# Kernel optimization log

Hardware: AMD Instinct MI355X
Metric: run time of the kernel (lower is better)

The kernel has to match this reference:

```python
import jax, jax.numpy as jnp
import numpy as np

B, S, D, H, DFF, PDIM = 16, 1024, 256, 8, 1024, 64
N = B * S
E = 262144
DH = D // H
EPS = 1e-5


def _ln(x, w=None, b=None):
    mu = jnp.mean(x, axis=-1, keepdims=True)
    var = jnp.mean((x - mu) ** 2, axis=-1, keepdims=True)
    xn = (x - mu) * jax.lax.rsqrt(var + EPS)
    if w is not None:
        xn = xn * w + b
    return xn


def setup_inputs() -> dict:
    key = jax.random.key(0)
    ks = jax.random.split(key, 24)
    sc = lambda *s: 0.02
    inp = {
        "x": jax.random.normal(ks[0], (B, S, D), jnp.float32),
        "prop_cond": jax.random.normal(ks[1], (B, PDIM), jnp.float32),
        "edge_index": jax.random.randint(ks[2], (2, E), 0, N, jnp.int64),
        # AdaLN 1 & 2
        "ada1_gw": jax.random.normal(ks[3], (D, PDIM)) * 0.02,
        "ada1_gb": jnp.ones((D,), jnp.float32),
        "ada1_bw": jax.random.normal(ks[4], (D, PDIM)) * 0.02,
        "ada1_bb": jnp.zeros((D,), jnp.float32),
        "ada2_gw": jax.random.normal(ks[5], (D, PDIM)) * 0.02,
        "ada2_gb": jnp.ones((D,), jnp.float32),
        "ada2_bw": jax.random.normal(ks[6], (D, PDIM)) * 0.02,
        "ada2_bb": jnp.zeros((D,), jnp.float32),
        # LayerNorms
        "ln1_w": jnp.ones((D,), jnp.float32), "ln1_b": jnp.zeros((D,), jnp.float32),
        "ln2_w": jnp.ones((D,), jnp.float32), "ln2_b": jnp.zeros((D,), jnp.float32),
        "gln_w": jnp.ones((D,), jnp.float32), "gln_b": jnp.zeros((D,), jnp.float32),
        # MHA
        "in_proj_w": jax.random.normal(ks[7], (3 * D, D)) * 0.02,
        "in_proj_b": jnp.zeros((3 * D,), jnp.float32),
        "out_proj_w": jax.random.normal(ks[8], (D, D)) * 0.02,
        "out_proj_b": jnp.zeros((D,), jnp.float32),
        # FFN
        "ffn_w1": jax.random.normal(ks[9], (DFF, D)) * 0.02,
        "ffn_b1": jnp.zeros((DFF,), jnp.float32),
        "ffn_w2": jax.random.normal(ks[10], (D, DFF)) * 0.02,
        "ffn_b2": jnp.zeros((D,), jnp.float32),
        # GATConv (heads=1, concat=False)
        "gat_w": jax.random.normal(ks[11], (D, D)) * 0.02,
        "gat_att_src": jax.random.normal(ks[12], (D,)) * 0.02,
        "gat_att_dst": jax.random.normal(ks[13], (D,)) * 0.02,
        "gat_bias": jnp.zeros((D,), jnp.float32),
    }
    return inp


def _forward(x, prop_cond, edge_index,
             ada1_gw, ada1_gb, ada1_bw, ada1_bb,
             ada2_gw, ada2_gb, ada2_bw, ada2_bb,
             ln1_w, ln1_b, ln2_w, ln2_b, gln_w, gln_b,
             in_proj_w, in_proj_b, out_proj_w, out_proj_b,
             ffn_w1, ffn_b1, ffn_w2, ffn_b2,
             gat_w, gat_att_src, gat_att_dst, gat_bias):
    # ---- AdaLN 1 + attention block ----
    residual = x
    gamma = (prop_cond @ ada1_gw.T + ada1_gb)[:, None, :]  # [B,1,D]
    beta = (prop_cond @ ada1_bw.T + ada1_bb)[:, None, :]
    xa = gamma * _ln(x) + beta
    xn = _ln(xa, ln1_w, ln1_b)
    qkv = xn @ in_proj_w.T + in_proj_b  # [B,S,3D]
    q, k, v = jnp.split(qkv, 3, axis=-1)
    q = q.reshape(B, S, H, DH)
    k = k.reshape(B, S, H, DH)
    v = v.reshape(B, S, H, DH)
    scores = jnp.einsum("bqhd,bkhd->bhqk", q, k) / jnp.sqrt(jnp.float32(DH))
    attn = jax.nn.softmax(scores, axis=-1)
    ao = jnp.einsum("bhqk,bkhd->bqhd", attn, v).reshape(B, S, D)
    ao = ao @ out_proj_w.T + out_proj_b
    x = residual + ao

    # ---- GATConv over flattened nodes (self-loops, leaky_relu 0.2) ----
    nodes = x.reshape(N, D)
    h = nodes @ gat_w.T  # [N,D]
    ar = jnp.arange(N, dtype=edge_index.dtype)
    src = jnp.concatenate([edge_index[0], ar])
    dst = jnp.concatenate([edge_index[1], ar])
    a_src = h @ gat_att_src  # [N]
    a_dst = h @ gat_att_dst
    e = jax.nn.leaky_relu(a_src[src] + a_dst[dst], 0.2)  # [E+N]
    m = jax.ops.segment_max(e, dst, num_segments=N)
    e = jnp.exp(e - m[dst])
    z = jax.ops.segment_sum(e, dst, num_segments=N)
    alpha = e / z[dst]
    agg = jax.ops.segment_sum(alpha[:, None] * h[src], dst, num_segments=N)
    gnn_out = (agg + gat_bias).reshape(B, S, D)
    x = x + gnn_out
    x = _ln(x, gln_w, gln_b)

    # ---- AdaLN 2 + FFN block ----
    residual = x
    gamma = (prop_cond @ ada2_gw.T + ada2_gb)[:, None, :]
    beta = (prop_cond @ ada2_bw.T + ada2_bb)[:, None, :]
    xa = gamma * _ln(x) + beta
    xn = _ln(xa, ln2_w, ln2_b)
    ff = jax.nn.gelu(xn @ ffn_w1.T + ffn_b1, approximate=False) @ ffn_w2.T + ffn_b2
    return residual + ff


def reference(x, prop_cond, edge_index,
              ada1_gw, ada1_gb, ada1_bw, ada1_bb,
              ada2_gw, ada2_gb, ada2_bw, ada2_bb,
              ln1_w, ln1_b, ln2_w, ln2_b, gln_w, gln_b,
              in_proj_w, in_proj_b, out_proj_w, out_proj_b,
              ffn_w1, ffn_b1, ffn_w2, ffn_b2,
              gat_w, gat_att_src, gat_att_dst, gat_bias):
    return _forward(x, prop_cond, edge_index,
                    ada1_gw, ada1_gb, ada1_bw, ada1_bb,
                    ada2_gw, ada2_gb, ada2_bw, ada2_bb,
                    ln1_w, ln1_b, ln2_w, ln2_b, gln_w, gln_b,
                    in_proj_w, in_proj_b, out_proj_w, out_proj_b,
                    ffn_w1, ffn_b1, ffn_w2, ffn_b2,
                    gat_w, gat_att_src, gat_att_dst, gat_bias)
```

## Files before the change

kernel.cpp:

```cpp
#include <hip/hip_runtime.h>
#include <cmath>

#define B_    16
#define S_    1024
#define D_    256
#define H_    8
#define DH_   32
#define DFF_  1024
#define PDIM_ 64
#define N_    (B_ * S_)
#define E_    262144
#define ETOT_ (E_ + N_)
#define EPS_  1e-5f

typedef __attribute__((ext_vector_type(8))) short bf16x8;
typedef __attribute__((ext_vector_type(4))) float f32x4;

__device__ __forceinline__ float wave_sum(float v) {
#pragma unroll
  for (int m = 1; m < 64; m <<= 1) v += __shfl_xor(v, m, 64);
  return v;
}
__device__ __forceinline__ float wave_max(float v) {
#pragma unroll
  for (int m = 1; m < 64; m <<= 1) v = fmaxf(v, __shfl_xor(v, m, 64));
  return v;
}

__device__ __forceinline__ unsigned short f2bf(float f) {
  unsigned int u = __float_as_uint(f);
  unsigned int r = u + 0x7fffu + ((u >> 16) & 1u);
  return (unsigned short)(r >> 16);
}
__device__ __forceinline__ float bf2f(unsigned short s) {
  return __uint_as_float(((unsigned int)s) << 16);
}
__device__ __forceinline__ void split4(float4 v, ushort4& hi, ushort4& lo) {
  unsigned short h;
  h = f2bf(v.x); hi.x = h; lo.x = f2bf(v.x - bf2f(h));
  h = f2bf(v.y); hi.y = h; lo.y = f2bf(v.y - bf2f(h));
  h = f2bf(v.z); hi.z = h; lo.z = f2bf(v.z - bf2f(h));
  h = f2bf(v.w); hi.w = h; lo.w = f2bf(v.w - bf2f(h));
}

__global__ __launch_bounds__(256) void gamma_beta_kernel(
    const float* __restrict__ pc,
    const float* __restrict__ g1w, const float* __restrict__ g1b,
    const float* __restrict__ b1w, const float* __restrict__ b1b,
    const float* __restrict__ g2w, const float* __restrict__ g2b,
    const float* __restrict__ b2w, const float* __restrict__ b2b,
    float* __restrict__ gamma1, float* __restrict__ beta1,
    float* __restrict__ gamma2, float* __restrict__ beta2) {
  int i = blockIdx.x * 256 + threadIdx.x;
  if (i >= B_ * D_) return;
  int b = i >> 8, d = i & 255;
  const float* p = pc + b * PDIM_;
  float s1 = 0.f, s2 = 0.f, s3 = 0.f, s4 = 0.f;
#pragma unroll 8
  for (int k = 0; k < PDIM_; ++k) {
    float pv = p[k];
    s1 += pv * g1w[d * PDIM_ + k];
    s2 += pv * b1w[d * PDIM_ + k];
    s3 += pv * g2w[d * PDIM_ + k];
    s4 += pv * b2w[d * PDIM_ + k];
  }
  gamma1[i] = s1 + g1b[d];
  beta1[i]  = s2 + b1b[d];
  gamma2[i] = s3 + g2b[d];
  beta2[i]  = s4 + b2b[d];
}

__global__ __launch_bounds__(256) void adaln_kernel(
    const float* __restrict__ x, const float* __restrict__ gamma,
    const float* __restrict__ beta, const float* __restrict__ lnw,
    const float* __restrict__ lnb, float* __restrict__ out) {
  int wid = threadIdx.x >> 6, lane = threadIdx.x & 63;
  int r = blockIdx.x * 4 + wid;
  int b = r >> 10;
  const int c = lane << 2;
  float4 v = *(const float4*)&x[(size_t)r * D_ + c];
  float sum = wave_sum(v.x + v.y + v.z + v.w);
  float mu = sum * (1.f / D_);
  float d0 = v.x - mu, d1 = v.y - mu, d2 = v.z - mu, d3 = v.w - mu;
  float sq = wave_sum(d0 * d0 + d1 * d1 + d2 * d2 + d3 * d3);
  float rs = rsqrtf(sq * (1.f / D_) + EPS_);
  float4 g  = *(const float4*)&gamma[b * D_ + c];
  float4 be = *(const float4*)&beta[b * D_ + c];
  float a0 = g.x * (d0 * rs) + be.x;
  float a1 = g.y * (d1 * rs) + be.y;
  float a2 = g.z * (d2 * rs) + be.z;
  float a3 = g.w * (d3 * rs) + be.w;
  float sum2 = wave_sum(a0 + a1 + a2 + a3);
  float mu2 = sum2 * (1.f / D_);
  float e0 = a0 - mu2, e1 = a1 - mu2, e2 = a2 - mu2, e3 = a3 - mu2;
  float sq2 = wave_sum(e0 * e0 + e1 * e1 + e2 * e2 + e3 * e3);
  float rs2 = rsqrtf(sq2 * (1.f / D_) + EPS_);
  float4 w  = *(const float4*)&lnw[c];
  float4 bb = *(const float4*)&lnb[c];
  float4 o;
  o.x = e0 * rs2 * w.x + bb.x;
  o.y = e1 * rs2 * w.y + bb.y;
  o.z = e2 * rs2 * w.z + bb.z;
  o.w = e3 * rs2 * w.w + bb.w;
  *(float4*)&out[(size_t)r * D_ + c] = o;
}

template <int EPI, int MS>
__global__ __launch_bounds__(256) void gemm_mfma_kernel(
    const float* __restrict__ A, const float* __restrict__ Wt,
    const float* __restrict__ bias, const float* __restrict__ R,
    float* __restrict__ C, int M, int Nc, int K) {
  __shared__ __align__(16) unsigned short Ah[MS * 32][40];
  __shared__ __align__(16) unsigned short Al[MS * 32][40];
  __shared__ __align__(16) unsigned short Bh[128][40];
  __shared__ __align__(16) unsigned short Bl[128][40];
  const int t = threadIdx.x;
  const int w = t >> 6, l = t & 63;
  const int lr = l & 15, lg = l >> 4;
  const int bm = blockIdx.y * (MS * 32), bn = blockIdx.x * 128;
  constexpr int SA = (MS == 4) ? 1 : 2;
  constexpr int NA = (MS == 4) ? 4 : 2;
  const int sra = t >> SA;
  const int ska = (t & ((1 << SA) - 1)) * (NA * 4);
  const int srb = t >> 1;
  const int skb = (t & 1) * 16;
  const float* Ap = A + (size_t)(bm + sra) * K + ska;
  const float* Bp = Wt + (size_t)(bn + srb) * K + skb;

  f32x4 acc[MS][4];
#pragma unroll
  for (int i = 0; i < MS; ++i)
#pragma unroll
    for (int j = 0; j < 4; ++j) acc[i][j] = (f32x4){0.f, 0.f, 0.f, 0.f};

  float4 ra[NA], rb[4];
#pragma unroll
  for (int c = 0; c < NA; ++c) ra[c] = *(const float4*)(Ap + c * 4);
#pragma unroll
  for (int c = 0; c < 4; ++c) rb[c] = *(const float4*)(Bp + c * 4);

  const int nk = K >> 5;
  for (int kt = 0; kt < nk; ++kt) {
    __syncthreads();
#pragma unroll
    for (int c = 0; c < NA; ++c) {
      ushort4 h4, l4;
      split4(ra[c], h4, l4);
      *(ushort4*)&Ah[sra][ska + c * 4] = h4;
      *(ushort4*)&Al[sra][ska + c * 4] = l4;
    }
#pragma unroll
    for (int c = 0; c < 4; ++c) {
      ushort4 h4, l4;
      split4(rb[c], h4, l4);
      *(ushort4*)&Bh[srb][skb + c * 4] = h4;
      *(ushort4*)&Bl[srb][skb + c * 4] = l4;
    }
    if (kt + 1 < nk) {
      Ap += 32;
      Bp += 32;
#pragma unroll
      for (int c = 0; c < NA; ++c) ra[c] = *(const float4*)(Ap + c * 4);
#pragma unroll
      for (int c = 0; c < 4; ++c) rb[c] = *(const float4*)(Bp + c * 4);
    }
    __syncthreads();
    bf16x8 bhj[4], blj[4];
#pragma unroll
    for (int j = 0; j < 4; ++j) {
      bhj[j] = *(const bf16x8*)&Bh[(w & 1) * 64 + j * 16 + lr][lg * 8];
      blj[j] = *(const bf16x8*)&Bl[(w & 1) * 64 + j * 16 + lr][lg * 8];
    }
#pragma unroll
    for (int i = 0; i < MS; ++i) {
      bf16x8 ahi = *(const bf16x8*)&Ah[(w >> 1) * (MS * 16) + i * 16 + lr][lg * 8];
      bf16x8 ali = *(const bf16x8*)&Al[(w >> 1) * (MS * 16) + i * 16 + lr][lg * 8];
#pragma unroll
      for (int j = 0; j < 4; ++j) {
        acc[i][j] = __builtin_amdgcn_mfma_f32_16x16x32_bf16(ahi, bhj[j], acc[i][j], 0, 0, 0);
        acc[i][j] = __builtin_amdgcn_mfma_f32_16x16x32_bf16(ali, bhj[j], acc[i][j], 0, 0, 0);
        acc[i][j] = __builtin_amdgcn_mfma_f32_16x16x32_bf16(ahi, blj[j], acc[i][j], 0, 0, 0);
      }
    }
  }
#pragma unroll
  for (int i = 0; i < MS; ++i) {
    const int m0 = bm + (w >> 1) * (MS * 16) + i * 16 + lg * 4;
#pragma unroll
    for (int j = 0; j < 4; ++j) {
      const int n = bn + (w & 1) * 64 + j * 16 + lr;
      const float bv = bias ? bias[n] : 0.f;
#pragma unroll
      for (int r = 0; r < 4; ++r) {
        const size_t idx = (size_t)(m0 + r) * Nc + n;
        float v = acc[i][j][r] + bv;
        if (EPI == 1) v = 0.5f * v * (1.f + erff(v * 0.7071067811865476f));
        if (EPI == 2) v += R[idx];
        C[idx] = v;
      }
    }
  }
}

__global__ __launch_bounds__(256) void attn_kernel(
    const float* __restrict__ qkv, float* __restrict__ ao) {
  __shared__ __align__(16) unsigned short Kh[64][40];
  __shared__ __align__(16) unsigned short Kl[64][40];
  __shared__ __align__(16) unsigned short VTh[32][72];
  __shared__ __align__(16) unsigned short VTl[32][72];
  __shared__ __align__(16) unsigned short Ph[4][16][72];
  __shared__ __align__(16) unsigned short Pl[4][16][72];

  const int t = threadIdx.x;
  const int w = t >> 6;
  const int l = t & 63;
  const int lq = l & 15;
  const int g = l >> 4;
  const int qt = blockIdx.x, h = blockIdx.y, b = blockIdx.z;
  const int qbase = qt * 256 + w * 64;

  const float QS = 0.2550332772677823f;

  bf16x8 qh[4], ql[4];
#pragma unroll
  for (int qs = 0; qs < 4; ++qs) {
    const size_t rowq =
        ((size_t)(b * S_ + qbase + qs * 16 + lq)) * 768 + h * DH_ + g * 8;
    float4 qa = *(const float4*)&qkv[rowq];
    float4 qb = *(const float4*)&qkv[rowq + 4];
    float qf[8] = {qa.x, qa.y, qa.z, qa.w, qb.x, qb.y, qb.z, qb.w};
#pragma unroll
    for (int j = 0; j < 8; ++j) {
      float f = qf[j] * QS;
      unsigned short hi = f2bf(f);
      qh[qs][j] = (short)hi;
      ql[qs][j] = (short)f2bf(f - bf2f(hi));
    }
  }

  f32x4 oacc[4][2];
  float mrun[4], lrun[4];
#pragma unroll
  for (int qs = 0; qs < 4; ++qs) {
    oacc[qs][0] = (f32x4){0.f, 0.f, 0.f, 0.f};
    oacc[qs][1] = (f32x4){0.f, 0.f, 0.f, 0.f};
    mrun[qs] = -1e30f;
    lrun[qs] = 0.f;
  }

  const int key_s = t >> 2;
  const int dg = t & 3;

  for (int kt = 0; kt < 16; ++kt) {
    __syncthreads();
    {
      const size_t rowb =
          ((size_t)(b * S_ + kt * 64 + key_s)) * 768 + h * DH_ + dg * 8;
      float4 ka = *(const float4*)&qkv[rowb + 256];
      float4 kb = *(const float4*)&qkv[rowb + 260];
      float4 va = *(const float4*)&qkv[rowb + 512];
      float4 vb = *(const float4*)&qkv[rowb + 516];
      ushort4 h0, h1, l0, l1;
      split4(ka, h0, l0);
      split4(kb, h1, l1);
      *(ushort4*)&Kh[key_s][dg * 8] = h0;
      *(ushort4*)&Kh[key_s][dg * 8 + 4] = h1;
      *(ushort4*)&Kl[key_s][dg * 8] = l0;
      *(ushort4*)&Kl[key_s][dg * 8 + 4] = l1;
      float vf[8] = {va.x, va.y, va.z, va.w, vb.x, vb.y, vb.z, vb.w};
#pragma unroll
      for (int j = 0; j < 8; ++j) {
        unsigned short vh = f2bf(vf[j]);
        VTh[dg * 8 + j][key_s] = vh;
        VTl[dg * 8 + j][key_s] = f2bf(vf[j] - bf2f(vh));
      }
    }
    __syncthreads();

    bf16x8 kfh[4], kfl[4];
#pragma unroll
    for (int i = 0; i < 4; ++i) {
      kfh[i] = *(const bf16x8*)&Kh[i * 16 + lq][g * 8];
      kfl[i] = *(const bf16x8*)&Kl[i * 16 + lq][g * 8];
    }

#pragma unroll
    for (int qs = 0; qs < 4; ++qs) {
      f32x4 s[4];
#pragma unroll
      for (int i = 0; i < 4; ++i) {
        f32x4 c = (f32x4){0.f, 0.f, 0.f, 0.f};
        c = __builtin_amdgcn_mfma_f32_16x16x32_bf16(kfh[i], qh[qs], c, 0, 0, 0);
        c = __builtin_amdgcn_mfma_f32_16x16x32_bf16(kfh[i], ql[qs], c, 0, 0, 0);
        c = __builtin_amdgcn_mfma_f32_16x16x32_bf16(kfl[i], qh[qs], c, 0, 0, 0);
        s[i] = c;
      }
      float pm = -1e30f;
#pragma unroll
      for (int i = 0; i < 4; ++i)
#pragma unroll
        for (int r = 0; r < 4; ++r) pm = fmaxf(pm, s[i][r]);
      pm = fmaxf(pm, __shfl_xor(pm, 16, 64));
      pm = fmaxf(pm, __shfl_xor(pm, 32, 64));
      float mnew = fmaxf(mrun[qs], pm);
      float rfac = exp2f(mrun[qs] - mnew);
      mrun[qs] = mnew;
      oacc[qs][0] *= rfac;
      oacc[qs][1] *= rfac;
      float lsum = 0.f;
#pragma unroll
      for (int i = 0; i < 4; ++i) {
        ushort4 hv, lv;
        unsigned short hr[4], lr4[4];
#pragma unroll
        for (int r = 0; r < 4; ++r) {
          float p = exp2f(s[i][r] - mnew);
          lsum += p;
          unsigned short ph = f2bf(p);
          hr[r] = ph;
          lr4[r] = f2bf(p - bf2f(ph));
        }
        hv.x = hr[0]; hv.y = hr[1]; hv.z = hr[2]; hv.w = hr[3];
        lv.x = lr4[0]; lv.y = lr4[1]; lv.z = lr4[2]; lv.w = lr4[3];
        *(ushort4*)&Ph[w][lq][i * 16 + g * 4] = hv;
        *(ushort4*)&Pl[w][lq][i * 16 + g * 4] = lv;
      }
      lsum += __shfl_xor(lsum, 16, 64);
      lsum += __shfl_xor(lsum, 32, 64);
      lrun[qs] = lrun[qs] * rfac + lsum;

#pragma unroll
      for (int kh2 = 0; kh2 < 2; ++kh2) {
        bf16x8 pb = *(const bf16x8*)&Ph[w][lq][kh2 * 32 + g * 8];
        bf16x8 pl = *(const bf16x8*)&Pl[w][lq][kh2 * 32 + g * 8];
#pragma unroll
        for (int d = 0; d < 2; ++d) {
          bf16x8 vh = *(const bf16x8*)&VTh[d * 16 + lq][kh2 * 32 + g * 8];
          bf16x8 vl = *(const bf16x8*)&VTl[d * 16 + lq][kh2 * 32 + g * 8];
          oacc[qs][d] = __builtin_amdgcn_mfma_f32_16x16x32_bf16(vh, pb, oacc[qs][d], 0, 0, 0);
          oacc[qs][d] = __builtin_amdgcn_mfma_f32_16x16x32_bf16(vh, pl, oacc[qs][d], 0, 0, 0);
          oacc[qs][d] = __builtin_amdgcn_mfma_f32_16x16x32_bf16(vl, pb, oacc[qs][d], 0, 0, 0);
        }
      }
    }
  }

#pragma unroll
  for (int qs = 0; qs < 4; ++qs) {
    float inv = 1.f / lrun[qs];
    const size_t orow =
        ((size_t)(b * S_ + qbase + qs * 16 + lq)) * D_ + h * DH_;
#pragma unroll
    for (int d = 0; d < 2; ++d) {
      float4 ov;
      ov.x = oacc[qs][d][0] * inv;
      ov.y = oacc[qs][d][1] * inv;
      ov.z = oacc[qs][d][2] * inv;
      ov.w = oacc[qs][d][3] * inv;
      *(float4*)&ao[orow + d * 16 + g * 4] = ov;
    }
  }
}

__global__ __launch_bounds__(256) void adot_kernel(
    const float* __restrict__ h, const float* __restrict__ att_src,
    const float* __restrict__ att_dst, float* __restrict__ a_src,
    float* __restrict__ a_dst) {
  int wid = threadIdx.x >> 6, lane = threadIdx.x & 63;
  int n = blockIdx.x * 4 + wid;
  const int c = lane << 2;
  float4 hv = *(const float4*)&h[(size_t)n * D_ + c];
  float4 as = *(const float4*)&att_src[c];
  float4 ad = *(const float4*)&att_dst[c];
  float s = hv.x * as.x + hv.y * as.y + hv.z * as.z + hv.w * as.w;
  float d = hv.x * ad.x + hv.y * ad.y + hv.z * ad.z + hv.w * ad.w;
  s = wave_sum(s);
  d = wave_sum(d);
  if (lane == 0) { a_src[n] = s; a_dst[n] = d; }
}

__global__ __launch_bounds__(256) void hist_kernel(
    const int* __restrict__ e_dst, int* __restrict__ counts) {
  int i = blockIdx.x * 256 + threadIdx.x;
  if (i >= ETOT_) return;
  int dst = (i < E_) ? e_dst[i] : (i - E_);
  atomicAdd(&counts[dst], 1);
}

__global__ __launch_bounds__(1024) void scan_kernel(
    const int* __restrict__ counts, int* __restrict__ offsets,
    int* __restrict__ cursor) {
  __shared__ int sums[1024];
  const int t = threadIdx.x;
  int local[16];
  int s = 0;
#pragma unroll
  for (int i = 0; i < 16; ++i) { local[i] = s; s += counts[t * 16 + i]; }
  sums[t] = s;
  __syncthreads();
  for (int off = 1; off < 1024; off <<= 1) {
    int v = (t >= off) ? sums[t - off] : 0;
    __syncthreads();
    sums[t] += v;
    __syncthreads();
  }
  int base = (t > 0) ? sums[t - 1] : 0;
#pragma unroll
  for (int i = 0; i < 16; ++i) {
    int o = base + local[i];
    offsets[t * 16 + i] = o;
    cursor[t * 16 + i] = o;
  }
  if (t == 1023) offsets[N_] = sums[1023];
}

__global__ __launch_bounds__(256) void scatter_kernel(
    const int* __restrict__ e_src, const int* __restrict__ e_dst,
    int* __restrict__ cursor, int* __restrict__ csr_src) {
  int i = blockIdx.x * 256 + threadIdx.x;
  if (i >= ETOT_) return;
  int s = (i < E_) ? e_src[i] : (i - E_);
  int d = (i < E_) ? e_dst[i] : (i - E_);
  int slot = atomicAdd(&cursor[d], 1);
  csr_src[slot] = s;
}

__global__ __launch_bounds__(256) void gat_ln_kernel(
    const float* __restrict__ h, const float* __restrict__ a_src,
    const float* __restrict__ a_dst, const int* __restrict__ offsets,
    const int* __restrict__ csr_src, const float* __restrict__ gat_bias,
    const float* __restrict__ x1, const float* __restrict__ gln_w,
    const float* __restrict__ gln_b, float* __restrict__ x2) {
  int wid = threadIdx.x >> 6, lane = threadIdx.x & 63;
  int n = blockIdx.x * 4 + wid;
  const int c = lane << 2;
  int beg = offsets[n], end = offsets[n + 1];
  float adn = a_dst[n];
  float m = -1e30f;
  for (int j = beg + lane; j < end; j += 64) {
    float e = a_src[csr_src[j]] + adn;
    e = (e >= 0.f) ? e : 0.2f * e;
    m = fmaxf(m, e);
  }
  m = wave_max(m);
  float z = 0.f;
  float ac0 = 0.f, ac1 = 0.f, ac2 = 0.f, ac3 = 0.f;
  for (int j0 = beg; j0 < end; j0 += 64) {
    int j = j0 + lane;
    float wgt = 0.f;
    int sidx = 0;
    if (j < end) {
      sidx = csr_src[j];
      float e = a_src[sidx] + adn;
      e = (e >= 0.f) ? e : 0.2f * e;
      wgt = __expf(e - m);
    }
    z += wgt;
    int cnt = min(64, end - j0);
    for (int jj = 0; jj < cnt; ++jj) {
      float ww = __shfl(wgt, jj, 64);
      int ss = __shfl(sidx, jj, 64);
      float4 hv = *(const float4*)&h[(size_t)ss * D_ + c];
      ac0 += ww * hv.x; ac1 += ww * hv.y; ac2 += ww * hv.z; ac3 += ww * hv.w;
    }
  }
  z = wave_sum(z);
  float inv = 1.f / z;
  float4 bv = *(const float4*)&gat_bias[c];
  float4 xv = *(const float4*)&x1[(size_t)n * D_ + c];
  float v0 = ac0 * inv + bv.x + xv.x;
  float v1 = ac1 * inv + bv.y + xv.y;
  float v2 = ac2 * inv + bv.z + xv.z;
  float v3 = ac3 * inv + bv.w + xv.w;
  float sum = wave_sum(v0 + v1 + v2 + v3);
  float mu = sum * (1.f / D_);
  float d0 = v0 - mu, d1 = v1 - mu, d2 = v2 - mu, d3 = v3 - mu;
  float sq = wave_sum(d0 * d0 + d1 * d1 + d2 * d2 + d3 * d3);
  float rs = rsqrtf(sq * (1.f / D_) + EPS_);
  float4 w4 = *(const float4*)&gln_w[c];
  float4 b4 = *(const float4*)&gln_b[c];
  float4 o;
  o.x = d0 * rs * w4.x + b4.x;
  o.y = d1 * rs * w4.y + b4.y;
  o.z = d2 * rs * w4.z + b4.z;
  o.w = d3 * rs * w4.w + b4.w;
  *(float4*)&x2[(size_t)n * D_ + c] = o;
}

extern "C" void kernel_launch(void* const* d_in, const int* in_sizes, int n_in,
                              void* d_out, int out_size, void* d_ws,
                              size_t ws_size, hipStream_t stream) {
  const float* x         = (const float*)d_in[0];
  const float* prop_cond = (const float*)d_in[1];
  const int*   edges     = (const int*)d_in[2];
  const float* a1gw = (const float*)d_in[3];
  const float* a1gb = (const float*)d_in[4];
  const float* a1bw = (const float*)d_in[5];
  const float* a1bb = (const float*)d_in[6];
  const float* a2gw = (const float*)d_in[7];
  const float* a2gb = (const float*)d_in[8];
  const float* a2bw = (const float*)d_in[9];
  const float* a2bb = (const float*)d_in[10];
  const float* ln1w = (const float*)d_in[11];
  const float* ln1b = (const float*)d_in[12];
  const float* ln2w = (const float*)d_in[13];
  const float* ln2b = (const float*)d_in[14];
  const float* glnw = (const float*)d_in[15];
  const float* glnb = (const float*)d_in[16];
  const float* ipw  = (const float*)d_in[17];
  const float* ipb  = (const float*)d_in[18];
  const float* opw  = (const float*)d_in[19];
  const float* opb  = (const float*)d_in[20];
  const float* f1w  = (const float*)d_in[21];
  const float* f1b  = (const float*)d_in[22];
  const float* f2w  = (const float*)d_in[23];
  const float* f2b  = (const float*)d_in[24];
  const float* gatw = (const float*)d_in[25];
  const float* gats = (const float*)d_in[26];
  const float* gatd = (const float*)d_in[27];
  const float* gatb = (const float*)d_in[28];
  float* out = (float*)d_out;

  const int* e_src = edges;
  const int* e_dst = edges + E_;

  float* W = (float*)d_ws;
  const size_t F_BIG = 0;
  const size_t F_XN  = F_BIG + 16777216;
  const size_t F_X1  = F_XN + 4194304;
  const size_t F_H   = F_X1 + 4194304;
  const size_t F_X2  = F_H + 4194304;
  const size_t F_GB  = F_X2 + 4194304;
  const size_t F_AS  = F_GB + 16384;
  const size_t F_AD  = F_AS + N_;
  const size_t F_INT = F_AD + N_;
  float* buf_big = W + F_BIG;
  float* buf_xn  = W + F_XN;
  float* buf_x1  = W + F_X1;
  float* buf_h   = W + F_H;
  float* buf_x2  = W + F_X2;
  float* gamma1  = W + F_GB;
  float* beta1   = gamma1 + 4096;
  float* gamma2  = beta1 + 4096;
  float* beta2   = gamma2 + 4096;
  float* a_src   = W + F_AS;
  float* a_dst   = W + F_AD;
  int* counts  = (int*)(W + F_INT);
  int* offsets = counts + N_;
  int* cursor  = offsets + N_ + 1;
  int* csr_src = cursor + N_;

  hipMemsetAsync(counts, 0, N_ * sizeof(int), stream);

  gamma_beta_kernel<<<16, 256, 0, stream>>>(prop_cond, a1gw, a1gb, a1bw, a1bb,
                                            a2gw, a2gb, a2bw, a2bb, gamma1,
                                            beta1, gamma2, beta2);
  adaln_kernel<<<N_ / 4, 256, 0, stream>>>(x, gamma1, beta1, ln1w, ln1b, buf_xn);
  gemm_mfma_kernel<0, 4><<<dim3(6, 128), 256, 0, stream>>>(
      buf_xn, ipw, ipb, nullptr, buf_big, N_, 768, 256);
  attn_kernel<<<dim3(4, 8, 16), 256, 0, stream>>>(buf_big, buf_xn);
  gemm_mfma_kernel<2, 2><<<dim3(2, 256), 256, 0, stream>>>(
      buf_xn, opw, opb, x, buf_x1, N_, 256, 256);
  gemm_mfma_kernel<0, 2><<<dim3(2, 256), 256, 0, stream>>>(
      buf_x1, gatw, nullptr, nullptr, buf_h, N_, 256, 256);
  adot_kernel<<<N_ / 4, 256, 0, stream>>>(buf_h, gats, gatd, a_src, a_dst);
  hist_kernel<<<(ETOT_ + 255) / 256, 256, 0, stream>>>(e_dst, counts);
  scan_kernel<<<1, 1024, 0, stream>>>(counts, offsets, cursor);
  scatter_kernel<<<(ETOT_ + 255) / 256, 256, 0, stream>>>(e_src, e_dst, cursor,
                                                          csr_src);
  gat_ln_kernel<<<N_ / 4, 256, 0, stream>>>(buf_h, a_src, a_dst, offsets,
                                            csr_src, gatb, buf_x1, glnw, glnb,
                                            buf_x2);
  adaln_kernel<<<N_ / 4, 256, 0, stream>>>(buf_x2, gamma2, beta2, ln2w, ln2b,
                                           buf_xn);
  gemm_mfma_kernel<1, 4><<<dim3(8, 128), 256, 0, stream>>>(
      buf_xn, f1w, f1b, nullptr, buf_big, N_, DFF_, 256);
  gemm_mfma_kernel<2, 2><<<dim3(2, 256), 256, 0, stream>>>(
      buf_big, f2w, f2b, buf_x2, out, N_, 256, DFF_);
}
```

Baseline: 534.5 us.

## Emit head-major split-bf16 QKV from GEMM epilogue and halve attention query tile

The QKV projection GEMM now writes its output as head-major panels of precomputed bf16 hi/lo pairs, with Q prescaled, instead of fp32 rows of 768. The attention kernel loads these halves directly, dropping its per-tile fp32-to-bf16 splitting and reading half the bytes for K/V. Each block also now covers 128 queries instead of 256, which doubles the grid to 1024 blocks for better occupancy but means K/V tiles are staged twice as often. The GEMM epilogue's scattered 2-byte stores may coalesce poorly.

```diff
diff --git a/kernel.cpp b/kernel.cpp
--- a/kernel.cpp
+++ b/kernel.cpp
@@ -14,7 +14,11 @@
 #define EPS_  1e-5f
 
 typedef __attribute__((ext_vector_type(8))) short bf16x8;
+typedef __attribute__((ext_vector_type(8))) unsigned short u16x8;
 typedef __attribute__((ext_vector_type(4))) float f32x4;
+
+#define QKV_SEC 8388608
+#define QKV_LO  4194304
 
 __device__ __forceinline__ float wave_sum(float v) {
 #pragma unroll
@@ -192,24 +196,37 @@
       const float bv = bias ? bias[n] : 0.f;
 #pragma unroll
       for (int r = 0; r < 4; ++r) {
-        const size_t idx = (size_t)(m0 + r) * Nc + n;
+        const int m = m0 + r;
         float v = acc[i][j][r] + bv;
-        if (EPI == 1) v = 0.5f * v * (1.f + erff(v * 0.7071067811865476f));
-        if (EPI == 2) v += R[idx];
-        C[idx] = v;
+        if constexpr (EPI == 3) {
+          const int sec = n >> 8, f = n & 255, hh = f >> 5, dd = f & 31;
+          if (sec == 0) v *= 0.2550332772677823f;
+          unsigned short hi = f2bf(v);
+          unsigned short lo = f2bf(v - bf2f(hi));
+          unsigned short* qs = (unsigned short*)C + (size_t)sec * QKV_SEC;
+          const size_t base =
+              ((size_t)((m >> 10) * H_ + hh) * S_ + (m & 1023)) * 32 + dd;
+          qs[base] = hi;
+          qs[base + QKV_LO] = lo;
+        } else {
+          const size_t idx = (size_t)m * Nc + n;
+          if constexpr (EPI == 1) v = 0.5f * v * (1.f + erff(v * 0.7071067811865476f));
+          if constexpr (EPI == 2) v += R[idx];
+          C[idx] = v;
+        }
       }
     }
   }
 }
 
 __global__ __launch_bounds__(256) void attn_kernel(
-    const float* __restrict__ qkv, float* __restrict__ ao) {
-  __shared__ __align__(16) unsigned short Kh[64][40];
-  __shared__ __align__(16) unsigned short Kl[64][40];
-  __shared__ __align__(16) unsigned short VTh[32][72];
-  __shared__ __align__(16) unsigned short VTl[32][72];
-  __shared__ __align__(16) unsigned short Ph[4][16][72];
-  __shared__ __align__(16) unsigned short Pl[4][16][72];
+    const unsigned short* __restrict__ qkvs, float* __restrict__ ao) {
+  __shared__ __align__(16) unsigned short KhL[64][40];
+  __shared__ __align__(16) unsigned short KlL[64][40];
+  __shared__ __align__(16) unsigned short VThL[32][72];
+  __shared__ __align__(16) unsigned short VTlL[32][72];
+  __shared__ __align__(16) unsigned short PhL[4][16][72];
+  __shared__ __align__(16) unsigned short PlL[4][16][72];
 
   const int t = threadIdx.x;
   const int w = t >> 6;
@@ -217,31 +234,28 @@
   const int lq = l & 15;
   const int g = l >> 4;
   const int qt = blockIdx.x, h = blockIdx.y, b = blockIdx.z;
-  const int qbase = qt * 256 + w * 64;
-
-  const float QS = 0.2550332772677823f;
-
-  bf16x8 qh[4], ql[4];
-#pragma unroll
-  for (int qs = 0; qs < 4; ++qs) {
-    const size_t rowq =
-        ((size_t)(b * S_ + qbase + qs * 16 + lq)) * 768 + h * DH_ + g * 8;
-    float4 qa = *(const float4*)&qkv[rowq];
-    float4 qb = *(const float4*)&qkv[rowq + 4];
-    float qf[8] = {qa.x, qa.y, qa.z, qa.w, qb.x, qb.y, qb.z, qb.w};
-#pragma unroll
-    for (int j = 0; j < 8; ++j) {
-      float f = qf[j] * QS;
-      unsigned short hi = f2bf(f);
-      qh[qs][j] = (short)hi;
-      ql[qs][j] = (short)f2bf(f - bf2f(hi));
-    }
-  }
-
-  f32x4 oacc[4][2];
-  float mrun[4], lrun[4];
-#pragma unroll
-  for (int qs = 0; qs < 4; ++qs) {
+  const int qbase = qt * 128 + w * 32;
+  const size_t panel = (size_t)(b * H_ + h) * S_;
+
+  const unsigned short* Qh_g = qkvs;
+  const unsigned short* Ql_g = qkvs + QKV_LO;
+  const unsigned short* Kh_g = qkvs + QKV_SEC;
+  const unsigned short* Kl_g = qkvs + QKV_SEC + QKV_LO;
+  const unsigned short* Vh_g = qkvs + 2 * QKV_SEC;
+  const unsigned short* Vl_g = qkvs + 2 * QKV_SEC + QKV_LO;
+
+  bf16x8 qh[2], ql[2];
+#pragma unroll
+  for (int qs = 0; qs < 2; ++qs) {
+    const size_t qi = (panel + qbase + qs * 16 + lq) * 32 + g * 8;
+    qh[qs] = *(const bf16x8*)&Qh_g[qi];
+    ql[qs] = *(const bf16x8*)&Ql_g[qi];
+  }
+
+  f32x4 oacc[2][2];
+  float mrun[2], lrun[2];
+#pragma unroll
+  for (int qs = 0; qs < 2; ++qs) {
     oacc[qs][0] = (f32x4){0.f, 0.f, 0.f, 0.f};
     oacc[qs][1] = (f32x4){0.f, 0.f, 0.f, 0.f};
     mrun[qs] = -1e30f;
@@ -254,25 +268,17 @@
   for (int kt = 0; kt < 16; ++kt) {
     __syncthreads();
     {
-      const size_t rowb =
-          ((size_t)(b * S_ + kt * 64 + key_s)) * 768 + h * DH_ + dg * 8;
-      float4 ka = *(const float4*)&qkv[rowb + 256];
-      float4 kb = *(const float4*)&qkv[rowb + 260];
-      float4 va = *(const float4*)&qkv[rowb + 512];
-      float4 vb = *(const float4*)&qkv[rowb + 516];
-      ushort4 h0, h1, l0, l1;
-      split4(ka, h0, l0);
-      split4(kb, h1, l1);
-      *(ushort4*)&Kh[key_s][dg * 8] = h0;
-      *(ushort4*)&Kh[key_s][dg * 8 + 4] = h1;
-      *(ushort4*)&Kl[key_s][dg * 8] = l0;
-      *(ushort4*)&Kl[key_s][dg * 8 + 4] = l1;
-      float vf[8] = {va.x, va.y, va.z, va.w, vb.x, vb.y, vb.z, vb.w};
+      const size_t kb = (panel + kt * 64 + key_s) * 32 + dg * 8;
+      u16x8 khv = *(const u16x8*)&Kh_g[kb];
+      u16x8 klv = *(const u16x8*)&Kl_g[kb];
+      *(u16x8*)&KhL[key_s][dg * 8] = khv;
+      *(u16x8*)&KlL[key_s][dg * 8] = klv;
+      u16x8 vhv = *(const u16x8*)&Vh_g[kb];
+      u16x8 vlv = *(const u16x8*)&Vl_g[kb];
 #pragma unroll
       for (int j = 0; j < 8; ++j) {
-        unsigned short vh = f2bf(vf[j]);
-        VTh[dg * 8 + j][key_s] = vh;
-        VTl[dg * 8 + j][key_s] = f2bf(vf[j] - bf2f(vh));
+        VThL[dg * 8 + j][key_s] = vhv[j];
+        VTlL[dg * 8 + j][key_s] = vlv[j];
       }
     }
     __syncthreads();
@@ -280,12 +286,12 @@
     bf16x8 kfh[4], kfl[4];
 #pragma unroll
     for (int i = 0; i < 4; ++i) {
-      kfh[i] = *(const bf16x8*)&Kh[i * 16 + lq][g * 8];
-      kfl[i] = *(const bf16x8*)&Kl[i * 16 + lq][g * 8];
-    }
-
-#pragma unroll
-    for (int qs = 0; qs < 4; ++qs) {
+      kfh[i] = *(const bf16x8*)&KhL[i * 16 + lq][g * 8];
+      kfl[i] = *(const bf16x8*)&KlL[i * 16 + lq][g * 8];
+    }
+
+#pragma unroll
+    for (int qs = 0; qs < 2; ++qs) {
       f32x4 s[4];
 #pragma unroll
       for (int i = 0; i < 4; ++i) {
@@ -322,8 +328,8 @@
         }
         hv.x = hr[0]; hv.y = hr[1]; hv.z = hr[2]; hv.w = hr[3];
         lv.x = lr4[0]; lv.y = lr4[1]; lv.z = lr4[2]; lv.w = lr4[3];
-        *(ushort4*)&Ph[w][lq][i * 16 + g * 4] = hv;
-        *(ushort4*)&Pl[w][lq][i * 16 + g * 4] = lv;
+        *(ushort4*)&PhL[w][lq][i * 16 + g * 4] = hv;
+        *(ushort4*)&PlL[w][lq][i * 16 + g * 4] = lv;
       }
       lsum += __shfl_xor(lsum, 16, 64);
       lsum += __shfl_xor(lsum, 32, 64);
@@ -331,12 +337,12 @@
 
 #pragma unroll
       for (int kh2 = 0; kh2 < 2; ++kh2) {
-        bf16x8 pb = *(const bf16x8*)&Ph[w][lq][kh2 * 32 + g * 8];
-        bf16x8 pl = *(const bf16x8*)&Pl[w][lq][kh2 * 32 + g * 8];
+        bf16x8 pb = *(const bf16x8*)&PhL[w][lq][kh2 * 32 + g * 8];
+        bf16x8 pl = *(const bf16x8*)&PlL[w][lq][kh2 * 32 + g * 8];
 #pragma unroll
         for (int d = 0; d < 2; ++d) {
-          bf16x8 vh = *(const bf16x8*)&VTh[d * 16 + lq][kh2 * 32 + g * 8];
-          bf16x8 vl = *(const bf16x8*)&VTl[d * 16 + lq][kh2 * 32 + g * 8];
+          bf16x8 vh = *(const bf16x8*)&VThL[d * 16 + lq][kh2 * 32 + g * 8];
+          bf16x8 vl = *(const bf16x8*)&VTlL[d * 16 + lq][kh2 * 32 + g * 8];
           oacc[qs][d] = __builtin_amdgcn_mfma_f32_16x16x32_bf16(vh, pb, oacc[qs][d], 0, 0, 0);
           oacc[qs][d] = __builtin_amdgcn_mfma_f32_16x16x32_bf16(vh, pl, oacc[qs][d], 0, 0, 0);
           oacc[qs][d] = __builtin_amdgcn_mfma_f32_16x16x32_bf16(vl, pb, oacc[qs][d], 0, 0, 0);
@@ -346,7 +352,7 @@
   }
 
 #pragma unroll
-  for (int qs = 0; qs < 4; ++qs) {
+  for (int qs = 0; qs < 2; ++qs) {
     float inv = 1.f / lrun[qs];
     const size_t orow =
         ((size_t)(b * S_ + qbase + qs * 16 + lq)) * D_ + h * DH_;
@@ -556,9 +562,10 @@
                                             a2gw, a2gb, a2bw, a2bb, gamma1,
                                             beta1, gamma2, beta2);
   adaln_kernel<<<N_ / 4, 256, 0, stream>>>(x, gamma1, beta1, ln1w, ln1b, buf_xn);
-  gemm_mfma_kernel<0, 4><<<dim3(6, 128), 256, 0, stream>>>(
+  gemm_mfma_kernel<3, 4><<<dim3(6, 128), 256, 0, stream>>>(
       buf_xn, ipw, ipb, nullptr, buf_big, N_, 768, 256);
-  attn_kernel<<<dim3(4, 8, 16), 256, 0, stream>>>(buf_big, buf_xn);
+  attn_kernel<<<dim3(8, 8, 16), 256, 0, stream>>>(
+      (const unsigned short*)buf_big, buf_xn);
   gemm_mfma_kernel<2, 2><<<dim3(2, 256), 256, 0, stream>>>(
       buf_xn, opw, opb, x, buf_x1, N_, 256, 256);
   gemm_mfma_kernel<0, 2><<<dim3(2, 256), 256, 0, stream>>>(
```

After: 491.9 us. -8.0%, faster.
